# Optimization experiments

Measured on AMD Instinct MI355X. Metric: run time of the kernel, lower is better.

The kernel has to match this reference:

```python
import jax, jax.numpy as jnp
import numpy as np

B, S, J, D = 64, 2048, 25, 3
FEAT_DIM = 128
COMPUTED = 12  # pos(3) + vel(3) + acc(3) + angles(3)
IN_MLP = COMPUTED * J  # 300
HID = FEAT_DIM * 2     # 256
CONN = np.array([(0, 1), (1, 5), (1, 6), (5, 7), (7, 9), (6, 8), (8, 10),
                 (1, 11), (1, 12), (11, 13), (13, 15), (12, 14), (14, 16)], dtype=np.int32)


def setup_inputs() -> dict:
    key = jax.random.key(0)
    ks = jax.random.split(key, 8)
    return {
        "poses": jax.random.normal(ks[0], (B, S, J, D), dtype=jnp.float32),
        "W1": jax.random.normal(ks[1], (IN_MLP, HID), dtype=jnp.float32) * 0.05,
        "b1": jnp.zeros((HID,), jnp.float32),
        "gamma": jnp.ones((HID,), jnp.float32),
        "beta": jnp.zeros((HID,), jnp.float32),
        "running_mean": jnp.zeros((HID,), jnp.float32),
        "running_var": jnp.ones((HID,), jnp.float32),
        "W2": jax.random.normal(ks[2], (HID, FEAT_DIM), dtype=jnp.float32) * 0.05,
        "b2": jnp.zeros((FEAT_DIM,), jnp.float32),
        "joint_weights": jnp.ones((J,), jnp.float32),
    }


def reference(poses, W1, b1, gamma, beta, running_mean, running_var, W2, b2, joint_weights):
    b, s, j, d = poses.shape
    # --- root-centering + max-distance normalization ---
    p = poses - poses[:, :, 0:1, :]
    dist = jnp.linalg.norm(p, axis=-1, keepdims=True)           # [B,S,J,1]
    max_dist = jnp.max(dist, axis=2, keepdims=True)             # [B,S,1,1]
    p = p / (max_dist + 1e-8)
    # --- velocity / acceleration (zero-padded first frames) ---
    zpad = jnp.zeros_like(p[:, :1])
    vel = jnp.concatenate([zpad, p[:, 1:] - p[:, :-1]], axis=1)
    acc = jnp.concatenate([zpad, vel[:, 1:] - vel[:, :-1]], axis=1)
    # --- joint angles: vectorized gather + normalize + acos (replaces B*S*13 python loop) ---
    v1 = p[:, :, CONN[:, 1], :] - p[:, :, CONN[:, 0], :]        # [B,S,13,3]
    vnorm = jnp.maximum(jnp.linalg.norm(v1, axis=-1, keepdims=True), 1e-12)  # F.normalize eps
    ang = jnp.arccos(jnp.clip(v1 / vnorm, -1.0, 1.0))           # [B,S,13,3]
    ang = ang.reshape(b, s, -1)                                 # [B,S,39]
    pad = jnp.zeros((b, s, j * 3 - ang.shape[-1]), ang.dtype)   # pad to J*3=75
    angles = jnp.concatenate([ang, pad], axis=-1).reshape(b, s, j, 3)
    # --- combine, weight, project ---
    feat = jnp.concatenate([p, vel, acc, angles], axis=-1)      # [B,S,J,12]
    feat = feat * joint_weights.reshape(1, 1, j, 1)
    x = feat.reshape(b * s, -1)                                 # [B*S,300]
    x = x @ W1 + b1
    x = gamma * (x - running_mean) / jnp.sqrt(running_var + 1e-5) + beta  # BN eval mode
    x = jax.nn.relu(x)                                          # dropout = identity (eval)
    x = x @ W2 + b2
    return x.reshape(b, s, -1)                                  # [B,S,128]
```

## Files before the change

kernel.cpp:

```cpp
#include <hip/hip_runtime.h>
#include <hip/hip_bf16.h>
#include <stdint.h>


#define S_    2048
#define MT_   64
#define TPB   512
#define HID_  256
#define OUT_  128

typedef __attribute__((ext_vector_type(8))) short   short8;
typedef __attribute__((ext_vector_type(4))) float   floatx4;

#define C0M 0x0ECDB118675110ULL
#define C1M 0x0FDECBA9786540ULL

__device__ __forceinline__ unsigned short bf16_bits(float v) {
    union { float f; unsigned u; } x; x.f = v;
    unsigned r = x.u + 0x7fffu + ((x.u >> 16) & 1u);
    return (unsigned short)(r >> 16);
}

__device__ __forceinline__ unsigned pkbf16(float a, float b) {
#if __has_builtin(__builtin_amdgcn_cvt_pk_bf16_f32)
    auto v = __builtin_amdgcn_cvt_pk_bf16_f32(a, b);
    unsigned u; __builtin_memcpy(&u, &v, 4); return u;
#else
    return (unsigned)bf16_bits(a) | ((unsigned)bf16_bits(b) << 16);
#endif
}

__device__ __forceinline__ float facos(float x) {
    float ax = fabsf(x);
    float p = fmaf(ax, -0.0187293f, 0.0742610f);
    p = fmaf(ax, p, -0.2121144f);
    p = fmaf(ax, p, 1.5707288f);
    float r = __builtin_amdgcn_sqrtf(1.f - ax) * p;
    return x < 0.f ? 3.14159265358979f - r : r;
}

__global__ void prep_kernel(const float* __restrict__ W1, const float* __restrict__ b1,
                            const float* __restrict__ gamma, const float* __restrict__ beta,
                            const float* __restrict__ rmean, const float* __restrict__ rvar,
                            const float* __restrict__ W2,
                            unsigned short* __restrict__ w1p,
                            unsigned short* __restrict__ w2p,
                            float* __restrict__ b1p) {
    int idx = blockIdx.x * 256 + threadIdx.x;
    if (idx < 81920) {
        int k = idx >> 8, n = idx & 255;
        float a = gamma[n] * __builtin_amdgcn_rsqf(rvar[n] + 1e-5f);
        float v = (k < 300) ? W1[k * HID_ + n] * a : 0.f;
        int blk = (k >> 5) * 16 + (n >> 4);
        int off = blk * 512 + (((k >> 3) & 3) * 16 + (n & 15)) * 8 + (k & 7);
        w1p[off] = bf16_bits(v);
    } else if (idx < 114688) {
        int i2 = idx - 81920;
        int k = i2 >> 7, n = i2 & 127;
        int blk = (k >> 5) * 8 + (n >> 4);
        int off = blk * 512 + (((k >> 3) & 3) * 16 + (n & 15)) * 8 + (k & 7);
        w2p[off] = bf16_bits(W2[k * OUT_ + n]);
    } else if (idx < 114944) {
        int n = idx - 114688;
        float a = gamma[n] * __builtin_amdgcn_rsqf(rvar[n] + 1e-5f);
        b1p[n] = fmaf(a, b1[n] - rmean[n], beta[n]);
    }
}

#define LDS_FEAT 0
#define LDS_PM   41984
#define LDS_RS   43312
#define LDS_JW   (LDS_RS + 66 * 16)
#define LDS_TOT  (LDS_JW + 25 * 4 + 12)

__global__ __launch_bounds__(TPB, 6) void pose_mlp(
    const float* __restrict__ poses,
    const unsigned short* __restrict__ w1p,
    const unsigned short* __restrict__ w2p,
    const float* __restrict__ b1p,
    const float* __restrict__ b2,
    const float* __restrict__ jw,
    float* __restrict__ out)
{
    __shared__ __align__(16) unsigned char smem[LDS_TOT];
    const int tid  = threadIdx.x;
    const int lane = tid & 63;
    const int wv   = tid >> 6;
    const int t0   = blockIdx.x * MT_;
    const int s0   = t0 & (S_ - 1);

    unsigned short* feat = (unsigned short*)(smem + LDS_FEAT);
    float*  pm  = (float*)(smem + LDS_PM);
    float4* rs  = (float4*)(smem + LDS_RS);
    float*  jwl = (float*)(smem + LDS_JW);

    short8 bw[2];
    #pragma unroll
    for (int ni = 0; ni < 2; ni++)
        bw[ni] = *(const short8*)(w1p + (unsigned)(wv * 2 + ni) * 512 + lane * 8);

    if (tid < 25) jwl[tid] = jw[tid];
    for (int i = tid; i < MT_ * 64; i += TPB) {
        int tt = i >> 6, z = i & 63;
        int k;
        if (z < 36) { int jj = z / 3; k = (13 + jj) * 12 + 9 + (z - jj * 3); }
        else        { k = 300 + z - 36; }
        feat[tt * 328 + k] = 0;
    }

    for (int i = tid; i < 66 * 5; i += TPB) {
        int f = i / 5, grp = i - f * 5;
        int g = t0 - 2 + f; if (g < 0) g = 0;
        const float* P = poses + (size_t)g * 75;
        float r0 = P[0], r1 = P[1], r2 = P[2];
        float m2 = 0.f;
        #pragma unroll
        for (int jj = 0; jj < 5; jj++) {
            int j = grp * 5 + jj;
            float dx = P[j*3]   - r0;
            float dy = P[j*3+1] - r1;
            float dz = P[j*3+2] - r2;
            m2 = fmaxf(m2, fmaf(dx, dx, fmaf(dy, dy, dz * dz)));
        }
        pm[i] = m2;
    }
    __syncthreads();
    if (tid < 66) {
        int g = t0 - 2 + tid; if (g < 0) g = 0;
        const float* P = poses + (size_t)g * 75;
        const float* q = pm + tid * 5;
        float m2 = fmaxf(fmaxf(fmaxf(q[0], q[1]), fmaxf(q[2], q[3])), q[4]);
        float sc = __builtin_amdgcn_rcpf(__builtin_amdgcn_sqrtf(m2) + 1e-8f);
        rs[tid] = make_float4(P[0], P[1], P[2], sc);
    }
    __syncthreads();

    for (int i = tid; i < MT_ * 25; i += TPB) {
        int tt = i / 25, j = i - tt * 25;
        int s  = s0 + tt;
        int g  = t0 + tt;
        int g1 = g - 1 < 0 ? 0 : g - 1;
        int g2 = g - 2 < 0 ? 0 : g - 2;
        const float* Pc = poses + (size_t)g  * 75 + j * 3;
        const float* P1 = poses + (size_t)g1 * 75 + j * 3;
        const float* P2 = poses + (size_t)g2 * 75 + j * 3;
        float4 rc = rs[tt + 2], rm = rs[tt + 1], rp = rs[tt];
        float cx = (Pc[0] - rc.x) * rc.w, cy = (Pc[1] - rc.y) * rc.w, cz = (Pc[2] - rc.z) * rc.w;
        float mx = (P1[0] - rm.x) * rm.w, my = (P1[1] - rm.y) * rm.w, mz = (P1[2] - rm.z) * rm.w;
        float px = (P2[0] - rp.x) * rp.w, py = (P2[1] - rp.y) * rp.w, pz = (P2[2] - rp.z) * rp.w;
        bool h1 = (s >= 1), h2 = (s >= 2);
        float vx = h1 ? cx - mx : 0.f, vy = h1 ? cy - my : 0.f, vz = h1 ? cz - mz : 0.f;
        float ux = h2 ? mx - px : 0.f, uy = h2 ? my - py : 0.f, uz = h2 ? mz - pz : 0.f;
        float qx = vx - ux, qy = vy - uy, qz = vz - uz;
        float w = jwl[j];
        unsigned base = (unsigned)tt * 328 + j * 12;
        *(unsigned*)(feat + base)     = pkbf16(cx * w, cy * w);
        *(unsigned*)(feat + base + 2) = pkbf16(cz * w, vx * w);
        *(unsigned*)(feat + base + 4) = pkbf16(vy * w, vz * w);
        *(unsigned*)(feat + base + 6) = pkbf16(qx * w, qy * w);
        feat[base + 8] = bf16_bits(qz * w);
    }

    for (int i = tid; i < MT_ * 13; i += TPB) {
        int tt = i / 13, e = i - tt * 13;
        int g  = t0 + tt;
        const float* P = poses + (size_t)g * 75;
        int a0 = (int)((C0M >> (4 * e)) & 15) * 3;
        int a1 = (((int)((C1M >> (4 * e)) & 15)) + 1) * 3;
        float vx = P[a1] - P[a0], vy = P[a1+1] - P[a0+1], vz = P[a1+2] - P[a0+2];
        float d  = fmaf(vx, vx, fmaf(vy, vy, vz * vz));
        float inv = __builtin_amdgcn_rcpf(fmaxf(__builtin_amdgcn_sqrtf(d), 1e-12f));
        float w = jwl[e];
        float A0 = facos(fminf(fmaxf(vx * inv, -1.f), 1.f)) * w;
        float A1 = facos(fminf(fmaxf(vy * inv, -1.f), 1.f)) * w;
        float A2 = facos(fminf(fmaxf(vz * inv, -1.f), 1.f)) * w;
        unsigned base = (unsigned)tt * 328 + e * 12 + 9;
        feat[base] = bf16_bits(A0);
        *(unsigned*)(feat + base + 1) = pkbf16(A1, A2);
    }
    __syncthreads();

    floatx4 acc[4][2];
    #pragma unroll
    for (int mi = 0; mi < 4; mi++)
        #pragma unroll
        for (int ni = 0; ni < 2; ni++) acc[mi][ni] = (floatx4){0.f, 0.f, 0.f, 0.f};

    #pragma unroll 1
    for (int kc = 0; kc < 10; kc++) {
        short8 bn[2];
        if (kc < 9) {
            #pragma unroll
            for (int ni = 0; ni < 2; ni++)
                bn[ni] = *(const short8*)(w1p + (unsigned)((kc + 1) * 16 + wv * 2 + ni) * 512 + lane * 8);
        }
        short8 af[4];
        #pragma unroll
        for (int mi = 0; mi < 4; mi++)
            af[mi] = *(const short8*)(feat + (mi * 16 + (lane & 15)) * 328 + kc * 32 + (lane >> 4) * 8);
        #pragma unroll
        for (int mi = 0; mi < 4; mi++)
            #pragma unroll
            for (int ni = 0; ni < 2; ni++)
                acc[mi][ni] = __builtin_amdgcn_mfma_f32_16x16x32_bf16(
                    af[mi], bw[ni], acc[mi][ni], 0, 0, 0);
        if (kc < 9) {
            #pragma unroll
            for (int ni = 0; ni < 2; ni++) bw[ni] = bn[ni];
        }
    }

    short8 bw2 = *(const short8*)(w2p + (unsigned)wv * 512 + lane * 8);

    __syncthreads();

    unsigned short* hid = feat;
    float bv[2];
    #pragma unroll
    for (int ni = 0; ni < 2; ni++) bv[ni] = b1p[wv * 32 + ni * 16 + (lane & 15)];
    #pragma unroll
    for (int mi = 0; mi < 4; mi++)
        #pragma unroll
        for (int ni = 0; ni < 2; ni++)
            #pragma unroll
            for (int r = 0; r < 4; r++) {
                float v = fmaxf(acc[mi][ni][r] + bv[ni], 0.f);
                int m   = mi * 16 + (lane >> 4) * 4 + r;
                int col = wv * 32 + ni * 16 + (lane & 15);
                hid[m * 264 + col] = bf16_bits(v);
            }
    __syncthreads();

    floatx4 acc2[4];
    #pragma unroll
    for (int mi = 0; mi < 4; mi++) acc2[mi] = (floatx4){0.f, 0.f, 0.f, 0.f};

    #pragma unroll 1
    for (int kc = 0; kc < 8; kc++) {
        short8 bn2;
        if (kc < 7)
            bn2 = *(const short8*)(w2p + (unsigned)((kc + 1) * 8 + wv) * 512 + lane * 8);
        short8 af[4];
        #pragma unroll
        for (int mi = 0; mi < 4; mi++)
            af[mi] = *(const short8*)(hid + (mi * 16 + (lane & 15)) * 264 + kc * 32 + (lane >> 4) * 8);
        #pragma unroll
        for (int mi = 0; mi < 4; mi++)
            acc2[mi] = __builtin_amdgcn_mfma_f32_16x16x32_bf16(
                af[mi], bw2, acc2[mi], 0, 0, 0);
        if (kc < 7) bw2 = bn2;
    }

    float c2 = b2[wv * 16 + (lane & 15)];
    #pragma unroll
    for (int mi = 0; mi < 4; mi++)
        #pragma unroll
        for (int r = 0; r < 4; r++) {
            int m   = mi * 16 + (lane >> 4) * 4 + r;
            int col = wv * 16 + (lane & 15);
            out[(size_t)(t0 + m) * OUT_ + col] = acc2[mi][r] + c2;
        }
}

extern "C" void kernel_launch(void* const* d_in, const int* in_sizes, int n_in,
                              void* d_out, int out_size, void* d_ws, size_t ws_size,
                              hipStream_t stream) {
    (void)in_sizes; (void)n_in; (void)out_size; (void)ws_size;
    const float* poses = (const float*)d_in[0];
    const float* W1    = (const float*)d_in[1];
    const float* b1    = (const float*)d_in[2];
    const float* gamma = (const float*)d_in[3];
    const float* beta  = (const float*)d_in[4];
    const float* rmean = (const float*)d_in[5];
    const float* rvar  = (const float*)d_in[6];
    const float* W2    = (const float*)d_in[7];
    const float* b2    = (const float*)d_in[8];
    const float* jw    = (const float*)d_in[9];

    unsigned short* w1p = (unsigned short*)d_ws;
    unsigned short* w2p = w1p + 320 * HID_;
    float* b1p = (float*)((char*)d_ws + (320 * HID_ + HID_ * OUT_) * 2);

    prep_kernel<<<449, 256, 0, stream>>>(W1, b1, gamma, beta, rmean, rvar, W2,
                                         w1p, w2p, b1p);
    pose_mlp<<<2048, TPB, 0, stream>>>(poses, w1p, w2p, b1p, b2, jw, (float*)d_out);
}
```

Baseline: 146.4 us.

## Fold velocity/acceleration into W1 and stage raw poses in LDS with fp16 MFMA

```diff
diff --git a/kernel.cpp b/kernel.cpp
--- a/kernel.cpp
+++ b/kernel.cpp
@@ -1,5 +1,4 @@
 #include <hip/hip_runtime.h>
-#include <hip/hip_bf16.h>
 #include <stdint.h>
 
 
@@ -8,27 +7,13 @@
 #define TPB   512
 #define HID_  256
 #define OUT_  128
-
-typedef __attribute__((ext_vector_type(8))) short   short8;
-typedef __attribute__((ext_vector_type(4))) float   floatx4;
+#define NTOK  131072
+
+typedef __attribute__((ext_vector_type(8))) _Float16 half8;
+typedef __attribute__((ext_vector_type(4))) float    floatx4;
 
 #define C0M 0x0ECDB118675110ULL
 #define C1M 0x0FDECBA9786540ULL
-
-__device__ __forceinline__ unsigned short bf16_bits(float v) {
-    union { float f; unsigned u; } x; x.f = v;
-    unsigned r = x.u + 0x7fffu + ((x.u >> 16) & 1u);
-    return (unsigned short)(r >> 16);
-}
-
-__device__ __forceinline__ unsigned pkbf16(float a, float b) {
-#if __has_builtin(__builtin_amdgcn_cvt_pk_bf16_f32)
-    auto v = __builtin_amdgcn_cvt_pk_bf16_f32(a, b);
-    unsigned u; __builtin_memcpy(&u, &v, 4); return u;
-#else
-    return (unsigned)bf16_bits(a) | ((unsigned)bf16_bits(b) << 16);
-#endif
-}
 
 __device__ __forceinline__ float facos(float x) {
     float ax = fabsf(x);
@@ -42,141 +27,146 @@
 __global__ void prep_kernel(const float* __restrict__ W1, const float* __restrict__ b1,
                             const float* __restrict__ gamma, const float* __restrict__ beta,
                             const float* __restrict__ rmean, const float* __restrict__ rvar,
-                            const float* __restrict__ W2,
-                            unsigned short* __restrict__ w1p,
-                            unsigned short* __restrict__ w2p,
+                            const float* __restrict__ W2, const float* __restrict__ jw,
+                            _Float16* __restrict__ w1p,
+                            _Float16* __restrict__ w2p,
                             float* __restrict__ b1p) {
     int idx = blockIdx.x * 256 + threadIdx.x;
-    if (idx < 81920) {
+    if (idx < 352 * 256) {
         int k = idx >> 8, n = idx & 255;
         float a = gamma[n] * __builtin_amdgcn_rsqf(rvar[n] + 1e-5f);
-        float v = (k < 300) ? W1[k * HID_ + n] * a : 0.f;
+        float v = 0.f;
+        if (k < 288) {
+            int d = k / 96, loc = k - d * 96;
+            if (loc < 75) {
+                int j = loc / 3, c = loc - j * 3;
+                const float* Wb = W1 + (j * 12 + c) * HID_ + n;
+                float wp = Wb[0], wv = Wb[3 * HID_], wa = Wb[6 * HID_];
+                float t = (d == 0) ? (wp + wv + wa) : (d == 1 ? -(wv + 2.f * wa) : wa);
+                v = t * a * jw[j];
+            }
+        } else {
+            int q = k - 288;
+            if (q < 39) {
+                int e = q / 3, aa = q - e * 3;
+                v = W1[(e * 12 + 9 + aa) * HID_ + n] * a * jw[e];
+            }
+        }
         int blk = (k >> 5) * 16 + (n >> 4);
         int off = blk * 512 + (((k >> 3) & 3) * 16 + (n & 15)) * 8 + (k & 7);
-        w1p[off] = bf16_bits(v);
-    } else if (idx < 114688) {
-        int i2 = idx - 81920;
+        w1p[off] = (_Float16)v;
+    } else if (idx < 352 * 256 + 256 * 128) {
+        int i2 = idx - 352 * 256;
         int k = i2 >> 7, n = i2 & 127;
         int blk = (k >> 5) * 8 + (n >> 4);
         int off = blk * 512 + (((k >> 3) & 3) * 16 + (n & 15)) * 8 + (k & 7);
-        w2p[off] = bf16_bits(W2[k * OUT_ + n]);
-    } else if (idx < 114944) {
-        int n = idx - 114688;
+        w2p[off] = (_Float16)W2[k * OUT_ + n];
+    } else if (idx < 352 * 256 + 256 * 128 + 256) {
+        int n = idx - (352 * 256 + 256 * 128);
         float a = gamma[n] * __builtin_amdgcn_rsqf(rvar[n] + 1e-5f);
         b1p[n] = fmaf(a, b1[n] - rmean[n], beta[n]);
     }
 }
 
-#define LDS_FEAT 0
-#define LDS_PM   41984
-#define LDS_RS   43312
-#define LDS_JW   (LDS_RS + 66 * 16)
-#define LDS_TOT  (LDS_JW + 25 * 4 + 12)
+#define L_CCB 0
+#define L_AB  13728
+#define L_RAW 22944
+#define L_RS  43424
+#define L_TOT 44480
 
 __global__ __launch_bounds__(TPB, 6) void pose_mlp(
     const float* __restrict__ poses,
-    const unsigned short* __restrict__ w1p,
-    const unsigned short* __restrict__ w2p,
+    const _Float16* __restrict__ w1p,
+    const _Float16* __restrict__ w2p,
     const float* __restrict__ b1p,
     const float* __restrict__ b2,
-    const float* __restrict__ jw,
     float* __restrict__ out)
 {
-    __shared__ __align__(16) unsigned char smem[LDS_TOT];
+    __shared__ __align__(16) unsigned char smem[L_TOT];
     const int tid  = threadIdx.x;
     const int lane = tid & 63;
     const int wv   = tid >> 6;
     const int t0   = blockIdx.x * MT_;
     const int s0   = t0 & (S_ - 1);
 
-    unsigned short* feat = (unsigned short*)(smem + LDS_FEAT);
-    float*  pm  = (float*)(smem + LDS_PM);
-    float4* rs  = (float4*)(smem + LDS_RS);
-    float*  jwl = (float*)(smem + LDS_JW);
-
-    short8 bw[2];
+    _Float16* ccb = (_Float16*)(smem + L_CCB);
+    _Float16* ab  = (_Float16*)(smem + L_AB);
+    float*    raw = (float*)(smem + L_RAW);
+    float4*   rs  = (float4*)(smem + L_RS);
+
+    half8 bw[2];
     #pragma unroll
     for (int ni = 0; ni < 2; ni++)
-        bw[ni] = *(const short8*)(w1p + (unsigned)(wv * 2 + ni) * 512 + lane * 8);
-
-    if (tid < 25) jwl[tid] = jw[tid];
-    for (int i = tid; i < MT_ * 64; i += TPB) {
-        int tt = i >> 6, z = i & 63;
-        int k;
-        if (z < 36) { int jj = z / 3; k = (13 + jj) * 12 + 9 + (z - jj * 3); }
-        else        { k = 300 + z - 36; }
-        feat[tt * 328 + k] = 0;
-    }
-
-    for (int i = tid; i < 66 * 5; i += TPB) {
-        int f = i / 5, grp = i - f * 5;
-        int g = t0 - 2 + f; if (g < 0) g = 0;
-        const float* P = poses + (size_t)g * 75;
-        float r0 = P[0], r1 = P[1], r2 = P[2];
+        bw[ni] = *(const half8*)(w1p + (unsigned)(wv * 2 + ni) * 512 + lane * 8);
+
+    #pragma unroll
+    for (int it = 0; it < 10; it++) {
+        int i = it * TPB + tid;
+        int src = t0 * 75 - 150 + i;
+        if (s0 == 0) { if (i < 75) src += 150; else if (i < 150) src += 75; }
+        src = src < NTOK * 75 - 1 ? src : NTOK * 75 - 1;
+        raw[i] = poses[src];
+    }
+    __syncthreads();
+
+    if (tid < 132) {
+        int f = tid >> 1, h = tid & 1;
+        const float* R = raw + f * 75;
+        float r0 = R[0], r1 = R[1], r2 = R[2];
         float m2 = 0.f;
         #pragma unroll
-        for (int jj = 0; jj < 5; jj++) {
-            int j = grp * 5 + jj;
-            float dx = P[j*3]   - r0;
-            float dy = P[j*3+1] - r1;
-            float dz = P[j*3+2] - r2;
-            m2 = fmaxf(m2, fmaf(dx, dx, fmaf(dy, dy, dz * dz)));
-        }
-        pm[i] = m2;
-    }
-    __syncthreads();
-    if (tid < 66) {
-        int g = t0 - 2 + tid; if (g < 0) g = 0;
-        const float* P = poses + (size_t)g * 75;
-        const float* q = pm + tid * 5;
-        float m2 = fmaxf(fmaxf(fmaxf(q[0], q[1]), fmaxf(q[2], q[3])), q[4]);
-        float sc = __builtin_amdgcn_rcpf(__builtin_amdgcn_sqrtf(m2) + 1e-8f);
-        rs[tid] = make_float4(P[0], P[1], P[2], sc);
-    }
-    __syncthreads();
-
-    for (int i = tid; i < MT_ * 25; i += TPB) {
-        int tt = i / 25, j = i - tt * 25;
-        int s  = s0 + tt;
-        int g  = t0 + tt;
-        int g1 = g - 1 < 0 ? 0 : g - 1;
-        int g2 = g - 2 < 0 ? 0 : g - 2;
-        const float* Pc = poses + (size_t)g  * 75 + j * 3;
-        const float* P1 = poses + (size_t)g1 * 75 + j * 3;
-        const float* P2 = poses + (size_t)g2 * 75 + j * 3;
-        float4 rc = rs[tt + 2], rm = rs[tt + 1], rp = rs[tt];
-        float cx = (Pc[0] - rc.x) * rc.w, cy = (Pc[1] - rc.y) * rc.w, cz = (Pc[2] - rc.z) * rc.w;
-        float mx = (P1[0] - rm.x) * rm.w, my = (P1[1] - rm.y) * rm.w, mz = (P1[2] - rm.z) * rm.w;
-        float px = (P2[0] - rp.x) * rp.w, py = (P2[1] - rp.y) * rp.w, pz = (P2[2] - rp.z) * rp.w;
-        bool h1 = (s >= 1), h2 = (s >= 2);
-        float vx = h1 ? cx - mx : 0.f, vy = h1 ? cy - my : 0.f, vz = h1 ? cz - mz : 0.f;
-        float ux = h2 ? mx - px : 0.f, uy = h2 ? my - py : 0.f, uz = h2 ? mz - pz : 0.f;
-        float qx = vx - ux, qy = vy - uy, qz = vz - uz;
-        float w = jwl[j];
-        unsigned base = (unsigned)tt * 328 + j * 12;
-        *(unsigned*)(feat + base)     = pkbf16(cx * w, cy * w);
-        *(unsigned*)(feat + base + 2) = pkbf16(cz * w, vx * w);
-        *(unsigned*)(feat + base + 4) = pkbf16(vy * w, vz * w);
-        *(unsigned*)(feat + base + 6) = pkbf16(qx * w, qy * w);
-        feat[base + 8] = bf16_bits(qz * w);
-    }
-
-    for (int i = tid; i < MT_ * 13; i += TPB) {
-        int tt = i / 13, e = i - tt * 13;
-        int g  = t0 + tt;
-        const float* P = poses + (size_t)g * 75;
-        int a0 = (int)((C0M >> (4 * e)) & 15) * 3;
-        int a1 = (((int)((C1M >> (4 * e)) & 15)) + 1) * 3;
-        float vx = P[a1] - P[a0], vy = P[a1+1] - P[a0+1], vz = P[a1+2] - P[a0+2];
-        float d  = fmaf(vx, vx, fmaf(vy, vy, vz * vz));
-        float inv = __builtin_amdgcn_rcpf(fmaxf(__builtin_amdgcn_sqrtf(d), 1e-12f));
-        float w = jwl[e];
-        float A0 = facos(fminf(fmaxf(vx * inv, -1.f), 1.f)) * w;
-        float A1 = facos(fminf(fmaxf(vy * inv, -1.f), 1.f)) * w;
-        float A2 = facos(fminf(fmaxf(vz * inv, -1.f), 1.f)) * w;
-        unsigned base = (unsigned)tt * 328 + e * 12 + 9;
-        feat[base] = bf16_bits(A0);
-        *(unsigned*)(feat + base + 1) = pkbf16(A1, A2);
+        for (int jj = 0; jj < 13; jj++) {
+            int j = h * 13 + jj;
+            if (j < 25) {
+                float dx = R[j * 3]     - r0;
+                float dy = R[j * 3 + 1] - r1;
+                float dz = R[j * 3 + 2] - r2;
+                m2 = fmaxf(m2, fmaf(dx, dx, fmaf(dy, dy, dz * dz)));
+            }
+        }
+        m2 = fmaxf(m2, __shfl_xor(m2, 1));
+        if (h == 0) {
+            float sc = __builtin_amdgcn_rcpf(__builtin_amdgcn_sqrtf(m2) + 1e-8f);
+            rs[f] = make_float4(r0, r1, r2, sc);
+        }
+    }
+    __syncthreads();
+
+    #pragma unroll 1
+    for (int i = tid; i < 66 * 32; i += TPB) {
+        int f = i >> 5, j = i & 31;
+        _Float16* C = ccb + f * 104;
+        if (j < 25) {
+            const float* R = raw + f * 75 + j * 3;
+            float4 q = rs[f];
+            C[j * 3 + 0] = (_Float16)((R[0] - q.x) * q.w);
+            C[j * 3 + 1] = (_Float16)((R[1] - q.y) * q.w);
+            C[j * 3 + 2] = (_Float16)((R[2] - q.z) * q.w);
+        } else {
+            int c = 75 + (j - 25) * 3;
+            C[c] = (_Float16)0.f; C[c + 1] = (_Float16)0.f; C[c + 2] = (_Float16)0.f;
+        }
+    }
+
+    #pragma unroll 1
+    for (int i = tid; i < 64 * 16; i += TPB) {
+        int tt = i >> 4, e = i & 15;
+        _Float16* A = ab + tt * 72;
+        if (e < 13) {
+            const float* R = raw + (tt + 2) * 75;
+            int a0 = (int)((C0M >> (4 * e)) & 15) * 3;
+            int a1 = (((int)((C1M >> (4 * e)) & 15)) + 1) * 3;
+            float vx = R[a1] - R[a0], vy = R[a1 + 1] - R[a0 + 1], vz = R[a1 + 2] - R[a0 + 2];
+            float d  = fmaf(vx, vx, fmaf(vy, vy, vz * vz));
+            float inv = __builtin_amdgcn_rcpf(fmaxf(__builtin_amdgcn_sqrtf(d), 1e-12f));
+            A[e * 3 + 0] = (_Float16)facos(fminf(fmaxf(vx * inv, -1.f), 1.f));
+            A[e * 3 + 1] = (_Float16)facos(fminf(fmaxf(vy * inv, -1.f), 1.f));
+            A[e * 3 + 2] = (_Float16)facos(fminf(fmaxf(vz * inv, -1.f), 1.f));
+        } else {
+            int c0 = 39 + (e - 13);
+            #pragma unroll
+            for (int k = 0; k < 9; k++) { int c = c0 + 3 * k; if (c < 64) A[c] = (_Float16)0.f; }
+        }
     }
     __syncthreads();
 
@@ -186,35 +176,63 @@
         #pragma unroll
         for (int ni = 0; ni < 2; ni++) acc[mi][ni] = (floatx4){0.f, 0.f, 0.f, 0.f};
 
+    unsigned rowb[4];
+    #pragma unroll
+    for (int mi = 0; mi < 4; mi++)
+        rowb[mi] = (unsigned)(mi * 16 + (lane & 15) + 2) * 104 + (lane >> 4) * 8;
+
+    int ko = 0, fofs = 0;
     #pragma unroll 1
-    for (int kc = 0; kc < 10; kc++) {
-        short8 bn[2];
-        if (kc < 9) {
+    for (int kc = 0; kc < 9; kc++) {
+        half8 bn[2];
+        #pragma unroll
+        for (int ni = 0; ni < 2; ni++)
+            bn[ni] = *(const half8*)(w1p + (unsigned)((kc + 1) * 16 + wv * 2 + ni) * 512 + lane * 8);
+        half8 af[4];
+        #pragma unroll
+        for (int mi = 0; mi < 4; mi++)
+            af[mi] = *(const half8*)(ccb + rowb[mi] + ko - fofs);
+        #pragma unroll
+        for (int mi = 0; mi < 4; mi++)
             #pragma unroll
             for (int ni = 0; ni < 2; ni++)
-                bn[ni] = *(const short8*)(w1p + (unsigned)((kc + 1) * 16 + wv * 2 + ni) * 512 + lane * 8);
-        }
-        short8 af[4];
-        #pragma unroll
-        for (int mi = 0; mi < 4; mi++)
-            af[mi] = *(const short8*)(feat + (mi * 16 + (lane & 15)) * 328 + kc * 32 + (lane >> 4) * 8);
-        #pragma unroll
-        for (int mi = 0; mi < 4; mi++)
-            #pragma unroll
-            for (int ni = 0; ni < 2; ni++)
-                acc[mi][ni] = __builtin_amdgcn_mfma_f32_16x16x32_bf16(
+                acc[mi][ni] = __builtin_amdgcn_mfma_f32_16x16x32_f16(
                     af[mi], bw[ni], acc[mi][ni], 0, 0, 0);
-        if (kc < 9) {
-            #pragma unroll
-            for (int ni = 0; ni < 2; ni++) bw[ni] = bn[ni];
-        }
-    }
-
-    short8 bw2 = *(const short8*)(w2p + (unsigned)wv * 512 + lane * 8);
-
-    __syncthreads();
-
-    unsigned short* hid = feat;
+        bw[0] = bn[0]; bw[1] = bn[1];
+        ko += 32; if (ko == 96) { ko = 0; fofs += 104; }
+    }
+    {
+        unsigned rowa[4];
+        #pragma unroll
+        for (int mi = 0; mi < 4; mi++)
+            rowa[mi] = (unsigned)(mi * 16 + (lane & 15)) * 72 + (lane >> 4) * 8;
+        #pragma unroll
+        for (int kc = 9; kc < 11; kc++) {
+            half8 bn[2];
+            if (kc < 10) {
+                #pragma unroll
+                for (int ni = 0; ni < 2; ni++)
+                    bn[ni] = *(const half8*)(w1p + (unsigned)((kc + 1) * 16 + wv * 2 + ni) * 512 + lane * 8);
+            }
+            half8 af[4];
+            #pragma unroll
+            for (int mi = 0; mi < 4; mi++)
+                af[mi] = *(const half8*)(ab + rowa[mi] + (kc - 9) * 32);
+            #pragma unroll
+            for (int mi = 0; mi < 4; mi++)
+                #pragma unroll
+                for (int ni = 0; ni < 2; ni++)
+                    acc[mi][ni] = __builtin_amdgcn_mfma_f32_16x16x32_f16(
+                        af[mi], bw[ni], acc[mi][ni], 0, 0, 0);
+            if (kc < 10) { bw[0] = bn[0]; bw[1] = bn[1]; }
+        }
+    }
+
+    half8 bw2 = *(const half8*)(w2p + (unsigned)wv * 512 + lane * 8);
+
+    __syncthreads();
+
+    _Float16* hid = (_Float16*)smem;
     float bv[2];
     #pragma unroll
     for (int ni = 0; ni < 2; ni++) bv[ni] = b1p[wv * 32 + ni * 16 + (lane & 15)];
@@ -227,7 +245,7 @@
                 float v = fmaxf(acc[mi][ni][r] + bv[ni], 0.f);
                 int m   = mi * 16 + (lane >> 4) * 4 + r;
                 int col = wv * 32 + ni * 16 + (lane & 15);
-                hid[m * 264 + col] = bf16_bits(v);
+                hid[m * 264 + col] = (_Float16)v;
             }
     __syncthreads();
 
@@ -237,16 +255,16 @@
 
     #pragma unroll 1
     for (int kc = 0; kc < 8; kc++) {
-        short8 bn2;
+        half8 bn2;
         if (kc < 7)
-            bn2 = *(const short8*)(w2p + (unsigned)((kc + 1) * 8 + wv) * 512 + lane * 8);
-        short8 af[4];
-        #pragma unroll
-        for (int mi = 0; mi < 4; mi++)
-            af[mi] = *(const short8*)(hid + (mi * 16 + (lane & 15)) * 264 + kc * 32 + (lane >> 4) * 8);
-        #pragma unroll
-        for (int mi = 0; mi < 4; mi++)
-            acc2[mi] = __builtin_amdgcn_mfma_f32_16x16x32_bf16(
+            bn2 = *(const half8*)(w2p + (unsigned)((kc + 1) * 8 + wv) * 512 + lane * 8);
+        half8 af[4];
+        #pragma unroll
+        for (int mi = 0; mi < 4; mi++)
+            af[mi] = *(const half8*)(hid + (mi * 16 + (lane & 15)) * 264 + kc * 32 + (lane >> 4) * 8);
+        #pragma unroll
+        for (int mi = 0; mi < 4; mi++)
+            acc2[mi] = __builtin_amdgcn_mfma_f32_16x16x32_f16(
                 af[mi], bw2, acc2[mi], 0, 0, 0);
         if (kc < 7) bw2 = bn2;
     }
@@ -277,11 +295,11 @@
     const float* b2    = (const float*)d_in[8];
     const float* jw    = (const float*)d_in[9];
 
-    unsigned short* w1p = (unsigned short*)d_ws;
-    unsigned short* w2p = w1p + 320 * HID_;
-    float* b1p = (float*)((char*)d_ws + (320 * HID_ + HID_ * OUT_) * 2);
-
-    prep_kernel<<<449, 256, 0, stream>>>(W1, b1, gamma, beta, rmean, rvar, W2,
+    _Float16* w1p = (_Float16*)d_ws;
+    _Float16* w2p = w1p + 352 * HID_;
+    float* b1p = (float*)((char*)d_ws + (352 * HID_ + HID_ * OUT_) * 2);
+
+    prep_kernel<<<481, 256, 0, stream>>>(W1, b1, gamma, beta, rmean, rvar, W2, jw,
                                          w1p, w2p, b1p);
-    pose_mlp<<<2048, TPB, 0, stream>>>(poses, w1p, w2p, b1p, b2, jw, (float*)d_out);
+    pose_mlp<<<2048, TPB, 0, stream>>>(poses, w1p, w2p, b1p, b2, (float*)d_out);
 }
```

After: 146.5 us. About the same (+0.1%).
